# Performance work log

Measured on AMD Instinct MI355X. Metric: run time of the kernel, lower is better.

Reference implementation:

```python
import jax, jax.numpy as jnp
import numpy as np

NUM_KNOTS = 64
HEAD_DIM = 4
SCALE = 0.5  # 1/sqrt(4)


def setup_inputs() -> dict:
    key = jax.random.key(0)
    ks = jax.random.split(key, 6)
    B, L, D = 4, 128, 256
    s = 1.0 / np.sqrt(D)
    return {
        "x": jax.random.normal(ks[0], (B, L, D), dtype=jnp.float32),
        "Wq": jax.random.normal(ks[1], (D, D), dtype=jnp.float32) * s,
        "Wk": jax.random.normal(ks[2], (D, D), dtype=jnp.float32) * s,
        "Wv": jax.random.normal(ks[3], (D, D), dtype=jnp.float32) * s,
        "Wo": jax.random.normal(ks[4], (D, D), dtype=jnp.float32) * s,
        "bo": jnp.zeros((D,), dtype=jnp.float32),
    }


def reference(x, Wq, Wk, Wv, Wo, bo):
    # x: [B, L, D], D = NUM_KNOTS * HEAD_DIM = 256
    B, L, D = x.shape
    N = L * NUM_KNOTS  # flattened 'knot' sequence length
    # nn.Linear applies x @ W.T
    q = (x @ Wq.T).reshape(B, N, HEAD_DIM)
    k = (x @ Wk.T).reshape(B, N, HEAD_DIM)
    v = (x @ Wv.T).reshape(B, N, HEAD_DIM)
    # full attention over the length-N knot sequence (head_dim = 4)
    logits = jnp.einsum("bnd,bmd->bnm", q, k) * SCALE  # [B, N, N]
    attn = jax.nn.softmax(logits, axis=-1)
    out = jnp.einsum("bnm,bmd->bnd", attn, v).reshape(B, L, D)
    return out @ Wo.T + bo
```

## Files before the change

kernel.cpp:

```cpp
#include <hip/hip_runtime.h>

#define NQ 8192
#define BLROWS 512
#define DIM 256
#define KSLICES 16

#define QSCALE 0.7213475204444817f

typedef float v2f __attribute__((ext_vector_type(2)));

__device__ __forceinline__ float ex2(float x) {
#if __has_builtin(__builtin_amdgcn_exp2f)
    return __builtin_amdgcn_exp2f(x);
#else
    return exp2f(x);
#endif
}

__global__ __launch_bounds__(256) void qkv_proj(
    const float* __restrict__ x,
    const float* __restrict__ Wq, const float* __restrict__ Wk,
    const float* __restrict__ Wv,
    float* __restrict__ Qb, float* __restrict__ Kb, float* __restrict__ Vb)
{
    const int m = blockIdx.y;
    const float* W = (m == 0) ? Wq : (m == 1) ? Wk : Wv;
    float* C       = (m == 0) ? Qb : (m == 1) ? Kb : Vb;
    const float sc = (m == 0) ? QSCALE : 1.0f;
    const int j  = threadIdx.x;
    const int rb = blockIdx.x * 4;

    float acc[4] = {0.f, 0.f, 0.f, 0.f};
    const float4* __restrict__ W4 = reinterpret_cast<const float4*>(W + j * DIM);
    const float*  __restrict__ A0 = x + rb * DIM;

    #pragma unroll 4
    for (int d4 = 0; d4 < DIM / 4; ++d4) {
        const float4 w = W4[d4];
        #pragma unroll
        for (int r = 0; r < 4; ++r) {
            const float4 a = reinterpret_cast<const float4*>(A0 + r * DIM)[d4];
            acc[r] = fmaf(a.x, w.x, acc[r]);
            acc[r] = fmaf(a.y, w.y, acc[r]);
            acc[r] = fmaf(a.z, w.z, acc[r]);
            acc[r] = fmaf(a.w, w.w, acc[r]);
        }
    }
    #pragma unroll
    for (int r = 0; r < 4; ++r)
        C[(rb + r) * DIM + j] = acc[r] * sc;
}

__global__ __launch_bounds__(256) void attn_partial(
    const float* __restrict__ Q, const float* __restrict__ K,
    const float* __restrict__ V, float* __restrict__ P)
{
    const int lane = threadIdx.x & 63;
    const int w    = __builtin_amdgcn_readfirstlane(threadIdx.x >> 6);
    const int qt   = blockIdx.x;
    const int ks   = blockIdx.y;
    const int b    = blockIdx.z;

    const float4* __restrict__ Qp = reinterpret_cast<const float4*>(Q) + b * NQ + qt * 256;
    const float4* __restrict__ Kp = reinterpret_cast<const float4*>(K) + b * NQ + ks * 512 + w * 128;
    const float4* __restrict__ Vp = reinterpret_cast<const float4*>(V) + b * NQ + ks * 512 + w * 128;

    v2f qx[2], qy[2], qz[2], qw[2];
    #pragma unroll
    for (int p = 0; p < 2; ++p) {
        const float4 t0 = Qp[(2 * p)     * 64 + lane];
        const float4 t1 = Qp[(2 * p + 1) * 64 + lane];
        qx[p] = v2f{t0.x, t1.x};
        qy[p] = v2f{t0.y, t1.y};
        qz[p] = v2f{t0.z, t1.z};
        qw[p] = v2f{t0.w, t1.w};
    }
    v2f a0[2], a1[2], a2[2], a3[2], ls[2];
    #pragma unroll
    for (int p = 0; p < 2; ++p) {
        a0[p] = v2f{0.f, 0.f}; a1[p] = v2f{0.f, 0.f};
        a2[p] = v2f{0.f, 0.f}; a3[p] = v2f{0.f, 0.f};
        ls[p] = v2f{0.f, 0.f};
    }

    #pragma unroll 8
    for (int j = 0; j < 128; ++j) {
        const float4 k4 = Kp[j];
        const float4 v4 = Vp[j];
        #pragma unroll
        for (int p = 0; p < 2; ++p) {
            v2f s = qx[p] * k4.x;
            s = __builtin_elementwise_fma(qy[p], v2f{k4.y, k4.y}, s);
            s = __builtin_elementwise_fma(qz[p], v2f{k4.z, k4.z}, s);
            s = __builtin_elementwise_fma(qw[p], v2f{k4.w, k4.w}, s);
            const v2f e = v2f{ex2(s[0]), ex2(s[1])};
            ls[p] += e;
            a0[p] = __builtin_elementwise_fma(e, v2f{v4.x, v4.x}, a0[p]);
            a1[p] = __builtin_elementwise_fma(e, v2f{v4.y, v4.y}, a1[p]);
            a2[p] = __builtin_elementwise_fma(e, v2f{v4.z, v4.z}, a2[p]);
            a3[p] = __builtin_elementwise_fma(e, v2f{v4.w, v4.w}, a3[p]);
        }
    }

    __shared__ float red[4][256][5];
    #pragma unroll
    for (int p = 0; p < 2; ++p) {
        #pragma unroll
        for (int e = 0; e < 2; ++e) {
            float* pr = &red[w][(2 * p + e) * 64 + lane][0];
            pr[0] = ls[p][e]; pr[1] = a0[p][e]; pr[2] = a1[p][e];
            pr[3] = a2[p][e]; pr[4] = a3[p][e];
        }
    }
    __syncthreads();

    float* __restrict__ Pb = P + (size_t)((b * KSLICES + ks) * 5) * NQ + qt * 256;
    const int qq = threadIdx.x;
    #pragma unroll
    for (int c = 0; c < 5; ++c) {
        const float sred = red[0][qq][c] + red[1][qq][c] + red[2][qq][c] + red[3][qq][c];
        Pb[c * NQ + qq] = sred;
    }
}

__global__ __launch_bounds__(256) void merge_oproj(
    const float* __restrict__ P, const float* __restrict__ Wo,
    const float* __restrict__ bo, float* __restrict__ out)
{
    __shared__ float aoL[4][DIM];

    const int rb = blockIdx.x * 4;
    const int b  = rb >> 7;
    const int n0 = (rb & 127) * 64;
    const int t  = threadIdx.x;

    {
        float sums[5] = {0.f, 0.f, 0.f, 0.f, 0.f};
        const float* __restrict__ Pb = P + (size_t)(b * KSLICES * 5) * NQ + n0 + t;
        #pragma unroll
        for (int s = 0; s < KSLICES; ++s) {
            #pragma unroll
            for (int c = 0; c < 5; ++c)
                sums[c] += Pb[(s * 5 + c) * NQ];
        }
        const float inv = 1.0f / sums[0];
        const int row = t >> 6;
        const int d0  = (t & 63) * 4;
        aoL[row][d0 + 0] = sums[1] * inv;
        aoL[row][d0 + 1] = sums[2] * inv;
        aoL[row][d0 + 2] = sums[3] * inv;
        aoL[row][d0 + 3] = sums[4] * inv;
    }
    __syncthreads();

    const int j = t;
    float acc[4] = {0.f, 0.f, 0.f, 0.f};
    const float4* __restrict__ W4 = reinterpret_cast<const float4*>(Wo + j * DIM);
    #pragma unroll 4
    for (int d4 = 0; d4 < DIM / 4; ++d4) {
        const float4 wv = W4[d4];
        #pragma unroll
        for (int r = 0; r < 4; ++r) {
            const float4 a = reinterpret_cast<const float4*>(&aoL[r][0])[d4];
            acc[r] = fmaf(a.x, wv.x, acc[r]);
            acc[r] = fmaf(a.y, wv.y, acc[r]);
            acc[r] = fmaf(a.z, wv.z, acc[r]);
            acc[r] = fmaf(a.w, wv.w, acc[r]);
        }
    }
    const float bias = bo[j];
    #pragma unroll
    for (int r = 0; r < 4; ++r)
        out[(rb + r) * DIM + j] = acc[r] + bias;
}

extern "C" void kernel_launch(void* const* d_in, const int* in_sizes, int n_in,
                              void* d_out, int out_size, void* d_ws, size_t ws_size,
                              hipStream_t stream) {
    const float* x  = (const float*)d_in[0];
    const float* Wq = (const float*)d_in[1];
    const float* Wk = (const float*)d_in[2];
    const float* Wv = (const float*)d_in[3];
    const float* Wo = (const float*)d_in[4];
    const float* bo = (const float*)d_in[5];
    float* out = (float*)d_out;

    float* Qb = (float*)d_ws;
    float* Kb = Qb + BLROWS * DIM;
    float* Vb = Kb + BLROWS * DIM;
    float* P  = Vb + BLROWS * DIM;

    qkv_proj<<<dim3(128, 3), 256, 0, stream>>>(x, Wq, Wk, Wv, Qb, Kb, Vb);
    attn_partial<<<dim3(32, KSLICES, 4), 256, 0, stream>>>(Qb, Kb, Vb, P);
    merge_oproj<<<128, 256, 0, stream>>>(P, Wo, bo, out);
}
```

Baseline: 86.90 us.

## Stage K/V slice in LDS and shrink reduction scratch with occupancy hint

```diff
diff --git a/kernel.cpp b/kernel.cpp
--- a/kernel.cpp
+++ b/kernel.cpp
@@ -51,20 +51,30 @@
         C[(rb + r) * DIM + j] = acc[r] * sc;
 }
 
-__global__ __launch_bounds__(256) void attn_partial(
+__global__ __launch_bounds__(256, 6) void attn_partial(
     const float* __restrict__ Q, const float* __restrict__ K,
     const float* __restrict__ V, float* __restrict__ P)
 {
-    const int lane = threadIdx.x & 63;
-    const int w    = __builtin_amdgcn_readfirstlane(threadIdx.x >> 6);
+    __shared__ float4 KV[1024];
+    __shared__ float  red2[4][256];
+
+    const int t    = threadIdx.x;
+    const int lane = t & 63;
+    const int w    = __builtin_amdgcn_readfirstlane(t >> 6);
     const int qt   = blockIdx.x;
     const int ks   = blockIdx.y;
     const int b    = blockIdx.z;
 
+    {
+        const float4* __restrict__ Kg = reinterpret_cast<const float4*>(K) + b * NQ + ks * 512;
+        const float4* __restrict__ Vg = reinterpret_cast<const float4*>(V) + b * NQ + ks * 512;
+        KV[t]             = Kg[t];
+        KV[t + 256]       = Kg[t + 256];
+        KV[512 + t]       = Vg[t];
+        KV[512 + t + 256] = Vg[t + 256];
+    }
+
     const float4* __restrict__ Qp = reinterpret_cast<const float4*>(Q) + b * NQ + qt * 256;
-    const float4* __restrict__ Kp = reinterpret_cast<const float4*>(K) + b * NQ + ks * 512 + w * 128;
-    const float4* __restrict__ Vp = reinterpret_cast<const float4*>(V) + b * NQ + ks * 512 + w * 128;
-
     v2f qx[2], qy[2], qz[2], qw[2];
     #pragma unroll
     for (int p = 0; p < 2; ++p) {
@@ -82,11 +92,15 @@
         a2[p] = v2f{0.f, 0.f}; a3[p] = v2f{0.f, 0.f};
         ls[p] = v2f{0.f, 0.f};
     }
-
-    #pragma unroll 8
+    __syncthreads();
+
+    const float4* __restrict__ Kl = &KV[w * 128];
+    const float4* __restrict__ Vl = &KV[512 + w * 128];
+
+    #pragma unroll 4
     for (int j = 0; j < 128; ++j) {
-        const float4 k4 = Kp[j];
-        const float4 v4 = Vp[j];
+        const float4 k4 = Kl[j];
+        const float4 v4 = Vl[j];
         #pragma unroll
         for (int p = 0; p < 2; ++p) {
             v2f s = qx[p] * k4.x;
@@ -102,25 +116,29 @@
         }
     }
 
-    __shared__ float red[4][256][5];
-    #pragma unroll
-    for (int p = 0; p < 2; ++p) {
-        #pragma unroll
-        for (int e = 0; e < 2; ++e) {
-            float* pr = &red[w][(2 * p + e) * 64 + lane][0];
-            pr[0] = ls[p][e]; pr[1] = a0[p][e]; pr[2] = a1[p][e];
-            pr[3] = a2[p][e]; pr[4] = a3[p][e];
-        }
-    }
+    float* __restrict__ Pb = P + (size_t)((b * KSLICES + ks) * 5) * NQ + qt * 256;
     __syncthreads();
 
-    float* __restrict__ Pb = P + (size_t)((b * KSLICES + ks) * 5) * NQ + qt * 256;
-    const int qq = threadIdx.x;
-    #pragma unroll
-    for (int c = 0; c < 5; ++c) {
-        const float sred = red[0][qq][c] + red[1][qq][c] + red[2][qq][c] + red[3][qq][c];
-        Pb[c * NQ + qq] = sred;
-    }
+#define RED_ROUND(ARR, cidx)                                              \
+    {                                                                     \
+        _Pragma("unroll")                                                 \
+        for (int p = 0; p < 2; ++p) {                                     \
+            _Pragma("unroll")                                             \
+            for (int e = 0; e < 2; ++e)                                   \
+                red2[w][(2 * p + e) * 64 + lane] = ARR[p][e];             \
+        }                                                                 \
+        __syncthreads();                                                  \
+        Pb[(cidx) * NQ + t] =                                             \
+            red2[0][t] + red2[1][t] + red2[2][t] + red2[3][t];            \
+        __syncthreads();                                                  \
+    }
+
+    RED_ROUND(ls, 0)
+    RED_ROUND(a0, 1)
+    RED_ROUND(a1, 2)
+    RED_ROUND(a2, 3)
+    RED_ROUND(a3, 4)
+#undef RED_ROUND
 }
 
 __global__ __launch_bounds__(256) void merge_oproj(
```

After: 91.56 us. 1.05x slower.

## Move attention core onto fp16 MFMA with hi/lo split-precision operands

Applied to the files above, without the earlier changes.

```diff
diff --git a/kernel.cpp b/kernel.cpp
--- a/kernel.cpp
+++ b/kernel.cpp
@@ -1,32 +1,32 @@
 #include <hip/hip_runtime.h>
+#include <stdint.h>
 
 #define NQ 8192
-#define BLROWS 512
 #define DIM 256
-#define KSLICES 16
+#define KSPLIT 8
 
 #define QSCALE 0.7213475204444817f
 
-typedef float v2f __attribute__((ext_vector_type(2)));
-
-__device__ __forceinline__ float ex2(float x) {
-#if __has_builtin(__builtin_amdgcn_exp2f)
-    return __builtin_amdgcn_exp2f(x);
-#else
-    return exp2f(x);
-#endif
+typedef _Float16 half8  __attribute__((ext_vector_type(8)));
+typedef float    f32x16 __attribute__((ext_vector_type(16)));
+
+union H8 { uint32_t u[4]; half8 h; };
+
+__device__ __forceinline__ float ex2(float x) { return __builtin_amdgcn_exp2f(x); }
+__device__ __forceinline__ uint32_t pkrtz(float a, float b) {
+    auto h = __builtin_amdgcn_cvt_pkrtz(a, b);
+    return __builtin_bit_cast(uint32_t, h);
 }
 
 __global__ __launch_bounds__(256) void qkv_proj(
     const float* __restrict__ x,
     const float* __restrict__ Wq, const float* __restrict__ Wk,
     const float* __restrict__ Wv,
-    float* __restrict__ Qb, float* __restrict__ Kb, float* __restrict__ Vb)
+    _Float16* __restrict__ Qh, _Float16* __restrict__ Kh,
+    _Float16* __restrict__ Vthi, _Float16* __restrict__ Vtlo)
 {
     const int m = blockIdx.y;
     const float* W = (m == 0) ? Wq : (m == 1) ? Wk : Wv;
-    float* C       = (m == 0) ? Qb : (m == 1) ? Kb : Vb;
-    const float sc = (m == 0) ? QSCALE : 1.0f;
     const int j  = threadIdx.x;
     const int rb = blockIdx.x * 4;
 
@@ -47,84 +47,136 @@
         }
     }
     #pragma unroll
-    for (int r = 0; r < 4; ++r)
-        C[(rb + r) * DIM + j] = acc[r] * sc;
-}
-
-__global__ __launch_bounds__(256) void attn_partial(
-    const float* __restrict__ Q, const float* __restrict__ K,
-    const float* __restrict__ V, float* __restrict__ P)
+    for (int r = 0; r < 4; ++r) {
+        const int rr = rb + r;
+        const int bb = rr >> 7, rowin = rr & 127;
+        const int n = rowin * 64 + (j >> 2), comp = j & 3;
+        if (m == 2) {
+            const _Float16 hi = (_Float16)acc[r];
+            const _Float16 lo = (_Float16)(acc[r] - (float)hi);
+            Vthi[((size_t)bb * 4 + comp) * NQ + n] = hi;
+            Vtlo[((size_t)bb * 4 + comp) * NQ + n] = lo;
+        } else {
+            const float v = (m == 0) ? acc[r] * QSCALE : acc[r];
+            const _Float16 hi = (_Float16)v;
+            const _Float16 lo = (_Float16)(v - (float)hi);
+            _Float16* dst = ((m == 0) ? Qh : Kh) + ((size_t)bb * NQ + n) * 8 + comp;
+            dst[0] = hi;
+            dst[4] = lo;
+        }
+    }
+}
+
+__global__ __launch_bounds__(256) void attn_mfma(
+    const _Float16* __restrict__ Qh, const _Float16* __restrict__ Kh,
+    const _Float16* __restrict__ Vthi, const _Float16* __restrict__ Vtlo,
+    float* __restrict__ Pp)
 {
-    const int lane = threadIdx.x & 63;
-    const int w    = __builtin_amdgcn_readfirstlane(threadIdx.x >> 6);
-    const int qt   = blockIdx.x;
-    const int ks   = blockIdx.y;
-    const int b    = blockIdx.z;
-
-    const float4* __restrict__ Qp = reinterpret_cast<const float4*>(Q) + b * NQ + qt * 256;
-    const float4* __restrict__ Kp = reinterpret_cast<const float4*>(K) + b * NQ + ks * 512 + w * 128;
-    const float4* __restrict__ Vp = reinterpret_cast<const float4*>(V) + b * NQ + ks * 512 + w * 128;
-
-    v2f qx[2], qy[2], qz[2], qw[2];
-    #pragma unroll
-    for (int p = 0; p < 2; ++p) {
-        const float4 t0 = Qp[(2 * p)     * 64 + lane];
-        const float4 t1 = Qp[(2 * p + 1) * 64 + lane];
-        qx[p] = v2f{t0.x, t1.x};
-        qy[p] = v2f{t0.y, t1.y};
-        qz[p] = v2f{t0.z, t1.z};
-        qw[p] = v2f{t0.w, t1.w};
-    }
-    v2f a0[2], a1[2], a2[2], a3[2], ls[2];
-    #pragma unroll
-    for (int p = 0; p < 2; ++p) {
-        a0[p] = v2f{0.f, 0.f}; a1[p] = v2f{0.f, 0.f};
-        a2[p] = v2f{0.f, 0.f}; a3[p] = v2f{0.f, 0.f};
-        ls[p] = v2f{0.f, 0.f};
-    }
-
-    #pragma unroll 8
-    for (int j = 0; j < 128; ++j) {
-        const float4 k4 = Kp[j];
-        const float4 v4 = Vp[j];
-        #pragma unroll
-        for (int p = 0; p < 2; ++p) {
-            v2f s = qx[p] * k4.x;
-            s = __builtin_elementwise_fma(qy[p], v2f{k4.y, k4.y}, s);
-            s = __builtin_elementwise_fma(qz[p], v2f{k4.z, k4.z}, s);
-            s = __builtin_elementwise_fma(qw[p], v2f{k4.w, k4.w}, s);
-            const v2f e = v2f{ex2(s[0]), ex2(s[1])};
-            ls[p] += e;
-            a0[p] = __builtin_elementwise_fma(e, v2f{v4.x, v4.x}, a0[p]);
-            a1[p] = __builtin_elementwise_fma(e, v2f{v4.y, v4.y}, a1[p]);
-            a2[p] = __builtin_elementwise_fma(e, v2f{v4.z, v4.z}, a2[p]);
-            a3[p] = __builtin_elementwise_fma(e, v2f{v4.w, v4.w}, a3[p]);
-        }
-    }
-
-    __shared__ float red[4][256][5];
-    #pragma unroll
-    for (int p = 0; p < 2; ++p) {
-        #pragma unroll
-        for (int e = 0; e < 2; ++e) {
-            float* pr = &red[w][(2 * p + e) * 64 + lane][0];
-            pr[0] = ls[p][e]; pr[1] = a0[p][e]; pr[2] = a1[p][e];
-            pr[3] = a2[p][e]; pr[4] = a3[p][e];
-        }
-    }
-    __syncthreads();
-
-    float* __restrict__ Pb = P + (size_t)((b * KSLICES + ks) * 5) * NQ + qt * 256;
-    const int qq = threadIdx.x;
-    #pragma unroll
-    for (int c = 0; c < 5; ++c) {
-        const float sred = red[0][qq][c] + red[1][qq][c] + red[2][qq][c] + red[3][qq][c];
-        Pb[c * NQ + qq] = sred;
+    const int t    = threadIdx.x;
+    const int w    = t >> 6;
+    const int lane = t & 63;
+    const int lo   = lane & 31, hi = lane >> 5;
+    const int qstrip = blockIdx.x * 4 + w;
+    const int ks     = blockIdx.y;
+    const int b      = blockIdx.z;
+    const int qbase  = qstrip * 32;
+    const int kbase  = ks * 1024;
+
+    H8 qhi, qlo;
+    {
+        uint4 qd = make_uint4(0, 0, 0, 0);
+        if (lane < 32)
+            qd = *reinterpret_cast<const uint4*>(Qh + ((size_t)b * NQ + qbase + lo) * 8);
+        qhi.u[0] = qd.x; qhi.u[1] = qd.y;
+        qhi.u[2] = (lane < 32) ? 0x00003C00u : 0u;
+        qhi.u[3] = 0;
+        qlo.u[0] = qd.z; qlo.u[1] = qd.w; qlo.u[2] = 0; qlo.u[3] = 0;
+    }
+    const _Float16* __restrict__ KhB = Kh + (size_t)b * NQ * 8;
+    const int c = lo;
+    const _Float16* __restrict__ VrowH = Vthi + ((size_t)b * 4 + (c < 4 ? c : 0)) * NQ;
+    const _Float16* __restrict__ VrowL = Vtlo + ((size_t)b * 4 + (c < 4 ? c : 0)) * NQ;
+
+    f32x16 acc = {};
+
+    auto LDK = [&](int kt) -> uint4 {
+        return (lane < 32)
+            ? *reinterpret_cast<const uint4*>(KhB + (size_t)(kt + lo) * 8)
+            : make_uint4(0, 0, 0, 0);
+    };
+    auto LDVH = [&](int kt) -> uint4 {
+        if (c < 4)  return *reinterpret_cast<const uint4*>(VrowH + kt + hi * 8);
+        if (c == 4) return make_uint4(0x3C003C00u, 0x3C003C00u, 0x3C003C00u, 0x3C003C00u);
+        return make_uint4(0, 0, 0, 0);
+    };
+    auto LDVL = [&](int kt) -> uint4 {
+        if (c < 4) return *reinterpret_cast<const uint4*>(VrowL + kt + hi * 8);
+        return make_uint4(0, 0, 0, 0);
+    };
+
+    uint4 kd  = LDK(kbase);
+    uint4 v1h = LDVH(kbase),      v1l = LDVL(kbase);
+    uint4 v2h = LDVH(kbase + 16), v2l = LDVL(kbase + 16);
+
+    #pragma unroll 1
+    for (int tt = 0; tt < 32; ++tt) {
+        uint4 kdn = kd, v1hn = v1h, v1ln = v1l, v2hn = v2h, v2ln = v2l;
+        if (tt < 31) {
+            const int kt2 = kbase + (tt + 1) * 32;
+            kdn = LDK(kt2);
+            v1hn = LDVH(kt2);      v1ln = LDVL(kt2);
+            v2hn = LDVH(kt2 + 16); v2ln = LDVL(kt2 + 16);
+        }
+
+        H8 ahi, alo;
+        ahi.u[0] = kd.x; ahi.u[1] = kd.y;
+        ahi.u[2] = (lane < 32) ? 0x0000C900u : 0u;
+        ahi.u[3] = 0;
+        alo.u[0] = kd.z; alo.u[1] = kd.w; alo.u[2] = 0; alo.u[3] = 0;
+        f32x16 z = {};
+        f32x16 S = __builtin_amdgcn_mfma_f32_32x32x16_f16(ahi.h, qhi.h, z, 0, 0, 0);
+        S = __builtin_amdgcn_mfma_f32_32x32x16_f16(ahi.h, qlo.h, S, 0, 0, 0);
+        S = __builtin_amdgcn_mfma_f32_32x32x16_f16(alo.h, qhi.h, S, 0, 0, 0);
+
+        float p[16];
+        #pragma unroll
+        for (int g = 0; g < 16; ++g) p[g] = ex2(S[g]);
+
+        uint32_t u0 = pkrtz(p[0], p[1]), u1 = pkrtz(p[2], p[3]);
+        uint32_t u2 = pkrtz(p[4], p[5]), u3 = pkrtz(p[6], p[7]);
+        asm("v_permlane32_swap_b32 %0, %1" : "+v"(u0), "+v"(u2));
+        asm("v_permlane32_swap_b32 %0, %1" : "+v"(u1), "+v"(u3));
+        H8 pf1; pf1.u[0] = u0; pf1.u[1] = u1; pf1.u[2] = u2; pf1.u[3] = u3;
+        H8 vf;
+        vf.u[0] = v1h.x; vf.u[1] = v1h.y; vf.u[2] = v1h.z; vf.u[3] = v1h.w;
+        acc = __builtin_amdgcn_mfma_f32_32x32x16_f16(vf.h, pf1.h, acc, 0, 0, 0);
+        vf.u[0] = v1l.x; vf.u[1] = v1l.y; vf.u[2] = v1l.z; vf.u[3] = v1l.w;
+        acc = __builtin_amdgcn_mfma_f32_32x32x16_f16(vf.h, pf1.h, acc, 0, 0, 0);
+
+        uint32_t u4 = pkrtz(p[8], p[9]),   u5 = pkrtz(p[10], p[11]);
+        uint32_t u6 = pkrtz(p[12], p[13]), u7 = pkrtz(p[14], p[15]);
+        asm("v_permlane32_swap_b32 %0, %1" : "+v"(u4), "+v"(u6));
+        asm("v_permlane32_swap_b32 %0, %1" : "+v"(u5), "+v"(u7));
+        H8 pf2; pf2.u[0] = u4; pf2.u[1] = u5; pf2.u[2] = u6; pf2.u[3] = u7;
+        vf.u[0] = v2h.x; vf.u[1] = v2h.y; vf.u[2] = v2h.z; vf.u[3] = v2h.w;
+        acc = __builtin_amdgcn_mfma_f32_32x32x16_f16(vf.h, pf2.h, acc, 0, 0, 0);
+        vf.u[0] = v2l.x; vf.u[1] = v2l.y; vf.u[2] = v2l.z; vf.u[3] = v2l.w;
+        acc = __builtin_amdgcn_mfma_f32_32x32x16_f16(vf.h, pf2.h, acc, 0, 0, 0);
+
+        kd = kdn; v1h = v1hn; v1l = v1ln; v2h = v2hn; v2l = v2ln;
+    }
+
+    float* __restrict__ Pb = Pp + (((size_t)(b * KSPLIT + ks)) * NQ + qbase) * 8;
+    if (lane < 32) {
+        *reinterpret_cast<float4*>(Pb + lo * 8) =
+            make_float4(acc[0], acc[1], acc[2], acc[3]);
+    } else {
+        Pb[lo * 8 + 4] = acc[0];
     }
 }
 
 __global__ __launch_bounds__(256) void merge_oproj(
-    const float* __restrict__ P, const float* __restrict__ Wo,
+    const float* __restrict__ Pp, const float* __restrict__ Wo,
     const float* __restrict__ bo, float* __restrict__ out)
 {
     __shared__ float aoL[4][DIM];
@@ -135,21 +187,23 @@
     const int t  = threadIdx.x;
 
     {
-        float sums[5] = {0.f, 0.f, 0.f, 0.f, 0.f};
-        const float* __restrict__ Pb = P + (size_t)(b * KSLICES * 5) * NQ + n0 + t;
-        #pragma unroll
-        for (int s = 0; s < KSLICES; ++s) {
-            #pragma unroll
-            for (int c = 0; c < 5; ++c)
-                sums[c] += Pb[(s * 5 + c) * NQ];
-        }
-        const float inv = 1.0f / sums[0];
+        const int n = n0 + t;
+        float4 num = make_float4(0.f, 0.f, 0.f, 0.f);
+        float den = 0.f;
+        #pragma unroll
+        for (int s = 0; s < KSPLIT; ++s) {
+            const float* q = Pp + (((size_t)(b * KSPLIT + s)) * NQ + n) * 8;
+            const float4 v4 = *reinterpret_cast<const float4*>(q);
+            num.x += v4.x; num.y += v4.y; num.z += v4.z; num.w += v4.w;
+            den += q[4];
+        }
+        const float inv = 1.0f / den;
         const int row = t >> 6;
         const int d0  = (t & 63) * 4;
-        aoL[row][d0 + 0] = sums[1] * inv;
-        aoL[row][d0 + 1] = sums[2] * inv;
-        aoL[row][d0 + 2] = sums[3] * inv;
-        aoL[row][d0 + 3] = sums[4] * inv;
+        aoL[row][d0 + 0] = num.x * inv;
+        aoL[row][d0 + 1] = num.y * inv;
+        aoL[row][d0 + 2] = num.z * inv;
+        aoL[row][d0 + 3] = num.w * inv;
     }
     __syncthreads();
 
@@ -185,12 +239,13 @@
     const float* bo = (const float*)d_in[5];
     float* out = (float*)d_out;
 
-    float* Qb = (float*)d_ws;
-    float* Kb = Qb + BLROWS * DIM;
-    float* Vb = Kb + BLROWS * DIM;
-    float* P  = Vb + BLROWS * DIM;
-
-    qkv_proj<<<dim3(128, 3), 256, 0, stream>>>(x, Wq, Wk, Wv, Qb, Kb, Vb);
-    attn_partial<<<dim3(32, KSLICES, 4), 256, 0, stream>>>(Qb, Kb, Vb, P);
-    merge_oproj<<<128, 256, 0, stream>>>(P, Wo, bo, out);
-}
+    _Float16* Qh   = (_Float16*)d_ws;
+    _Float16* Kh   = Qh + 4 * NQ * 8;
+    _Float16* Vthi = Kh + 4 * NQ * 8;
+    _Float16* Vtlo = Vthi + 4 * 4 * NQ;
+    float*    Pp   = (float*)(Vtlo + 4 * 4 * NQ);
+
+    qkv_proj<<<dim3(128, 3), 256, 0, stream>>>(x, Wq, Wk, Wv, Qh, Kh, Vthi, Vtlo);
+    attn_mfma<<<dim3(64, KSPLIT, 4), 256, 0, stream>>>(Qh, Kh, Vthi, Vtlo, Pp);
+    merge_oproj<<<128, 256, 0, stream>>>(Pp, Wo, bo, out);
+}
```

Result: slower. 102.2 us (+17.6%).
